# Performance work log

Measured on AMD Instinct MI355X. Metric: run time of the kernel, lower is better.

Reference implementation:

```python
import jax, jax.numpy as jnp
import numpy as np


def phi(x):
    return jax.nn.elu(x) + 1.0


def setup_inputs() -> dict:
    key = jax.random.key(0)
    ks = jax.random.split(key, 6)
    B, C, H, W = 16, 256, 64, 64
    scale = 1.0 / np.sqrt(C)
    x = jax.random.normal(ks[0], (B, C, H, W), dtype=jnp.float32)
    Wq = jax.random.normal(ks[1], (C, C), dtype=jnp.float32) * scale
    Wk = jax.random.normal(ks[2], (C, C), dtype=jnp.float32) * scale
    Wv = jax.random.normal(ks[3], (C, C), dtype=jnp.float32) * scale
    Wo = jax.random.normal(ks[4], (C, C), dtype=jnp.float32) * scale
    bo = jnp.zeros((C,), dtype=jnp.float32)
    return {"x": x, "Wq": Wq, "Wk": Wk, "Wv": Wv, "Wo": Wo, "bo": bo}


def reference(x, Wq, Wk, Wv, Wo, bo):
    # 1x1 convs == channel matmuls: out[b,o,h,w] = sum_c W[o,c] x[b,c,h,w]
    q = jnp.einsum('oc,bchw->bohw', Wq, x)
    k = jnp.einsum('oc,bchw->bohw', Wk, x)
    v = jnp.einsum('oc,bchw->bohw', Wv, x)
    phi_q, phi_k, phi_v = phi(q), phi(k), phi(v)
    # context matrix per batch: [B, C, C]
    qv = jnp.einsum('bchw,bdhw->bcd', phi_q, phi_v)
    # per-batch 1x1 conv with weight qv[b] applied to phi_k[b]
    attended = jnp.einsum('bcd,bdhw->bchw', qv, phi_k)
    # output projection with bias; dropout is identity at eval
    out = jnp.einsum('oc,bchw->bohw', Wo, attended) + bo[None, :, None, None]
    return out
```

## Files before the change

### kernel.cpp

```cpp
#include <hip/hip_runtime.h>
#include <hip/hip_bf16.h>


typedef short  bf16x8 __attribute__((ext_vector_type(8)));
typedef float  f32x4  __attribute__((ext_vector_type(4)));
typedef unsigned short u16x4 __attribute__((ext_vector_type(4)));

#define NB 16
#define NC 256
#define NN 4096

__device__ __forceinline__ unsigned short f2bf(float f) {
    union { float f; unsigned u; } v; v.f = f;
    unsigned r = v.u + 0x7FFFu + ((v.u >> 16) & 1u);
    return (unsigned short)(r >> 16);
}

__device__ __forceinline__ float phi_act(float v) {
    return v > 0.f ? v + 1.f : __expf(v);
}

__device__ __forceinline__ void gload_lds16(const void* g, void* l) {
    __builtin_amdgcn_global_load_lds(
        (const __attribute__((address_space(1))) void*)g,
        (__attribute__((address_space(3))) void*)l, 16, 0, 0);
}

__device__ __forceinline__ void stage_tile(
    const unsigned short* __restrict__ src, int ld, int kb, char* lds, int t)
{
    const int kslot  = t & 7;
    const int rbase  = t >> 3;
    const int srcOff = (kslot * 16) ^ ((rbase & 7) << 4);
    const int wbase  = (t >> 6) * 1024;
    #pragma unroll
    for (int i = 0; i < 4; ++i) {
        const int r = i * 32 + rbase;
        const char* g = (const char*)(src + (size_t)r * ld + kb) + srcOff;
        gload_lds16(g, lds + i * 4096 + wbase);
    }
}

__device__ __forceinline__ bf16x8 frag_ld(const char* lds, int row, int kbyte) {
    return *(const bf16x8*)(lds + row * 128 + (kbyte ^ ((row & 7) << 4)));
}

template<bool SWAP>
__device__ __forceinline__ void gemm128(
    const unsigned short* __restrict__ A, int lda,
    const unsigned short* __restrict__ BT, int ldb,
    int k0, int nk, char* lsA, char* lsB, f32x4 (&acc)[4][4])
{
    const int t = threadIdx.x;
    const int lane = t & 63;
    const int w  = t >> 6;
    const int wr = (w >> 1) * 64, wc = (w & 1) * 64;
    const int q  = lane >> 4, c15 = lane & 15;

    for (int kt = 0; kt < nk; ++kt) {
        const int kb = k0 + kt * 64;
        if (kt) __syncthreads();
        stage_tile(A,  lda, kb, lsA, t);
        stage_tile(BT, ldb, kb, lsB, t);
        __syncthreads();
        #pragma unroll
        for (int g = 0; g < 2; ++g) {
            const int kbyte = g * 64 + q * 16;
            bf16x8 af[4], bfr[4];
            #pragma unroll
            for (int m = 0; m < 4; ++m) af[m]  = frag_ld(lsA, wr + m * 16 + c15, kbyte);
            #pragma unroll
            for (int n = 0; n < 4; ++n) bfr[n] = frag_ld(lsB, wc + n * 16 + c15, kbyte);
            #pragma unroll
            for (int m = 0; m < 4; ++m)
                #pragma unroll
                for (int n = 0; n < 4; ++n)
                    acc[m][n] = SWAP
                        ? __builtin_amdgcn_mfma_f32_16x16x32_bf16(bfr[n], af[m], acc[m][n], 0, 0, 0)
                        : __builtin_amdgcn_mfma_f32_16x16x32_bf16(af[m], bfr[n], acc[m][n], 0, 0, 0);
        }
    }
}

__global__ __launch_bounds__(256) void k_wconv(
    const float* __restrict__ Wq, const float* __restrict__ Wk,
    const float* __restrict__ Wv, const float* __restrict__ Wo,
    unsigned short* __restrict__ Wqkv, unsigned short* __restrict__ Wob)
{
    int i = blockIdx.x * 256 + threadIdx.x;
    if      (i < 65536)  Wqkv[i] = f2bf(Wq[i]);
    else if (i < 131072) Wqkv[i] = f2bf(Wk[i - 65536]);
    else if (i < 196608) Wqkv[i] = f2bf(Wv[i - 131072]);
    else if (i < 262144) Wob[i - 196608] = f2bf(Wo[i - 196608]);
}

__global__ __launch_bounds__(256) void k_xpose(
    const float* __restrict__ x, unsigned short* __restrict__ xT)
{
    __shared__ float tile[64][68];
    const int b  = blockIdx.z;
    const int n0 = blockIdx.x * 64, c0 = blockIdx.y * 64;
    const int t  = threadIdx.x;
    const float* xp = x + ((size_t)b * NC + c0) * NN + n0;
    const int cc = t >> 4, nq = t & 15;
    #pragma unroll
    for (int j = 0; j < 4; ++j) {
        const int c = j * 16 + cc;
        f32x4 v = *(const f32x4*)(xp + (size_t)c * NN + nq * 4);
        *(f32x4*)&tile[c][nq * 4] = v;
    }
    __syncthreads();
    unsigned short* op = xT + ((size_t)b * NN + n0) * NC + c0;
    const int nn0 = t >> 4, cq = t & 15;
    #pragma unroll
    for (int j = 0; j < 4; ++j) {
        const int nn = j * 16 + nn0;
        u16x4 o;
        #pragma unroll
        for (int ii = 0; ii < 4; ++ii) o[ii] = f2bf(tile[cq * 4 + ii][nn]);
        *(u16x4*)(op + (size_t)nn * NC + cq * 4) = o;
    }
}

__global__ __launch_bounds__(256) void k_proj(
    const unsigned short* __restrict__ Wqkv, const unsigned short* __restrict__ xT,
    unsigned short* __restrict__ phiQ, unsigned short* __restrict__ phiKT,
    unsigned short* __restrict__ phiV)
{
    __shared__ char lds[32768];
    const int bid = blockIdx.x;
    const int nt  = bid & 31;
    const int mt  = (bid >> 5) % 6;
    const int b   = bid / 192;
    const unsigned short* A  = Wqkv + mt * 128 * NC;
    const unsigned short* BT = xT + ((size_t)b * NN + nt * 128) * NC;

    const int lane = threadIdx.x & 63;
    const int w    = threadIdx.x >> 6;
    const int wr   = (w >> 1) * 64, wc = (w & 1) * 64;
    const int q4   = (lane >> 4) * 4, c15 = lane & 15;
    const int p    = mt >> 1;

    f32x4 acc[4][4] = {};
    if (p == 1) {
        gemm128<false>(A, NC, BT, NC, 0, 4, lds, lds + 16384, acc);
        unsigned short* dst = phiKT + (size_t)b * NN * NC;
        const int cb = (mt & 1) * 128 + wr + q4;
        const int nb = nt * 128 + wc + c15;
        #pragma unroll
        for (int m = 0; m < 4; ++m)
            #pragma unroll
            for (int n = 0; n < 4; ++n) {
                u16x4 pk;
                #pragma unroll
                for (int i = 0; i < 4; ++i) pk[i] = f2bf(phi_act(acc[m][n][i]));
                *(u16x4*)(dst + (size_t)(nb + n * 16) * NC + cb + m * 16) = pk;
            }
    } else {
        gemm128<true>(A, NC, BT, NC, 0, 4, lds, lds + 16384, acc);
        unsigned short* dst = (p == 0 ? phiQ : phiV) + (size_t)b * NC * NN;
        const int ob = (mt & 1) * 128 + wr + c15;
        const int nb = nt * 128 + wc + q4;
        #pragma unroll
        for (int m = 0; m < 4; ++m)
            #pragma unroll
            for (int n = 0; n < 4; ++n) {
                u16x4 pk;
                #pragma unroll
                for (int i = 0; i < 4; ++i) pk[i] = f2bf(phi_act(acc[m][n][i]));
                *(u16x4*)(dst + (size_t)(ob + m * 16) * NN + nb + n * 16) = pk;
            }
    }
}

__global__ __launch_bounds__(256) void k_qv(
    const unsigned short* __restrict__ phiQ, const unsigned short* __restrict__ phiV,
    float* __restrict__ qvTp)
{
    __shared__ char lds[32768];
    const int bid = blockIdx.x;
    const int s = bid & 7, nt = (bid >> 3) & 1, mt = (bid >> 4) & 1, b = bid >> 5;
    const unsigned short* A  = phiQ + ((size_t)b * NC + mt * 128) * NN;
    const unsigned short* BT = phiV + ((size_t)b * NC + nt * 128) * NN;
    f32x4 acc[4][4] = {};
    gemm128<false>(A, NN, BT, NN, s * 512, 8, lds, lds + 16384, acc);

    const int lane = threadIdx.x & 63, w = threadIdx.x >> 6;
    const int wr = (w >> 1) * 64, wc = (w & 1) * 64;
    const int q4 = (lane >> 4) * 4, c15 = lane & 15;
    float* dst = qvTp + (((size_t)s * NB + b) << 16);
    const int c0 = mt * 128 + wr + q4;
    const int d0 = nt * 128 + wc + c15;
    #pragma unroll
    for (int m = 0; m < 4; ++m)
        #pragma unroll
        for (int n = 0; n < 4; ++n)
            *(f32x4*)(dst + (size_t)(d0 + n * 16) * NC + c0 + m * 16) = acc[m][n];
}

__global__ __launch_bounds__(256) void k_qvred(
    const float* __restrict__ p, unsigned short* __restrict__ qvT)
{
    const size_t i = (size_t)blockIdx.x * 256 + threadIdx.x;
    const f32x4* pv = (const f32x4*)p;
    f32x4 v = pv[i];
    #pragma unroll
    for (int s = 1; s < 8; ++s) v = v + pv[i + (size_t)s * 262144];
    u16x4 o;
    #pragma unroll
    for (int j = 0; j < 4; ++j) o[j] = f2bf(v[j]);
    ((u16x4*)qvT)[i] = o;
}

__global__ __launch_bounds__(256) void k_mproj(
    const unsigned short* __restrict__ Wob, const unsigned short* __restrict__ qvT,
    unsigned short* __restrict__ Mb)
{
    __shared__ char lds[32768];
    const int bid = blockIdx.x;
    const int nt = bid & 1, mt = (bid >> 1) & 1, b = bid >> 2;
    const unsigned short* A  = Wob + mt * 128 * NC;
    const unsigned short* BT = qvT + ((size_t)b << 16) + nt * 128 * NC;
    f32x4 acc[4][4] = {};
    gemm128<true>(A, NC, BT, NC, 0, 4, lds, lds + 16384, acc);

    const int lane = threadIdx.x & 63, w = threadIdx.x >> 6;
    const int wr = (w >> 1) * 64, wc = (w & 1) * 64;
    const int q4 = (lane >> 4) * 4, c15 = lane & 15;
    unsigned short* dst = Mb + ((size_t)b << 16);
    const int ob = mt * 128 + wr + c15;
    const int db = nt * 128 + wc + q4;
    #pragma unroll
    for (int m = 0; m < 4; ++m)
        #pragma unroll
        for (int n = 0; n < 4; ++n) {
            u16x4 pk;
            #pragma unroll
            for (int i = 0; i < 4; ++i) pk[i] = f2bf(acc[m][n][i]);
            *(u16x4*)(dst + (size_t)(ob + m * 16) * NC + db + n * 16) = pk;
        }
}

__global__ __launch_bounds__(256) void k_out(
    const unsigned short* __restrict__ Mb, const unsigned short* __restrict__ phiKT,
    const float* __restrict__ bo, float* __restrict__ out)
{
    __shared__ char lds[32768];
    const int bid = blockIdx.x;
    const int nt = bid & 31, mt = (bid >> 5) & 1, b = bid >> 6;
    const unsigned short* A  = Mb + ((size_t)b << 16) + mt * 128 * NC;
    const unsigned short* BT = phiKT + (size_t)b * NN * NC + (size_t)nt * 128 * NC;
    f32x4 acc[4][4] = {};
    gemm128<true>(A, NC, BT, NC, 0, 4, lds, lds + 16384, acc);

    const int lane = threadIdx.x & 63, w = threadIdx.x >> 6;
    const int wr = (w >> 1) * 64, wc = (w & 1) * 64;
    const int q4 = (lane >> 4) * 4, c15 = lane & 15;
    float* dst = out + (size_t)b * NC * NN;
    #pragma unroll
    for (int m = 0; m < 4; ++m) {
        const int o  = mt * 128 + wr + m * 16 + c15;
        const float bb = bo[o];
        #pragma unroll
        for (int n = 0; n < 4; ++n) {
            f32x4 v = acc[m][n];
            #pragma unroll
            for (int i = 0; i < 4; ++i) v[i] += bb;
            *(f32x4*)(dst + (size_t)o * NN + nt * 128 + wc + n * 16 + q4) = v;
        }
    }
}

extern "C" void kernel_launch(void* const* d_in, const int* in_sizes, int n_in,
                              void* d_out, int out_size, void* d_ws, size_t ws_size,
                              hipStream_t stream)
{
    (void)in_sizes; (void)n_in; (void)out_size; (void)ws_size;
    const float* x  = (const float*)d_in[0];
    const float* Wq = (const float*)d_in[1];
    const float* Wk = (const float*)d_in[2];
    const float* Wv = (const float*)d_in[3];
    const float* Wo = (const float*)d_in[4];
    const float* bo = (const float*)d_in[5];
    float* out = (float*)d_out;

    char* ws = (char*)d_ws;
    size_t off = 0;
    auto alloc = [&](size_t bytes) {
        void* p = ws + off;
        off += (bytes + 255) & ~(size_t)255;
        return p;
    };
    unsigned short* xT    = (unsigned short*)alloc((size_t)NB * NN * NC * 2);
    unsigned short* phiQ  = (unsigned short*)alloc((size_t)NB * NC * NN * 2);
    unsigned short* phiV  = (unsigned short*)alloc((size_t)NB * NC * NN * 2);
    unsigned short* phiKT = (unsigned short*)alloc((size_t)NB * NN * NC * 2);
    unsigned short* qvT   = (unsigned short*)alloc((size_t)NB * NC * NC * 2);
    unsigned short* Mb    = (unsigned short*)alloc((size_t)NB * NC * NC * 2);
    unsigned short* Wqkv  = (unsigned short*)alloc((size_t)768 * NC * 2);
    unsigned short* Wob   = (unsigned short*)alloc((size_t)NC * NC * 2);
    float* qvTp = (float*)xT;

    k_wconv<<<1024, 256, 0, stream>>>(Wq, Wk, Wv, Wo, Wqkv, Wob);
    k_xpose<<<dim3(NN / 64, NC / 64, NB), dim3(256), 0, stream>>>(x, xT);
    k_proj<<<NB * 6 * 32, 256, 0, stream>>>(Wqkv, xT, phiQ, phiKT, phiV);
    k_qv<<<NB * 2 * 2 * 8, 256, 0, stream>>>(phiQ, phiV, qvTp);
    k_qvred<<<1024, 256, 0, stream>>>(qvTp, qvT);
    k_mproj<<<NB * 2 * 2, 256, 0, stream>>>(Wob, qvT, Mb);
    k_out<<<NB * 2 * 32, 256, 0, stream>>>(Mb, phiKT, bo, out);
}
```

Before: 126.4 us.

## Keep weight tiles in registers and double-buffer LDS staging across GEMM kernels

Adds a GEMM helper that loads the full K=256 A operand (weights or the M matrix) into registers once, then streams several 128-column B tiles through double-buffered LDS, running an epilogue per tile. k_proj is split into separate QV and K kernels, each covering several N tiles per block, and k_out/k_mproj use the same helper. k_qv switches to a double-buffered LDS pipeline so the next tile loads while MFMAs run on the current one. Together these cut redundant A reloads and barrier stalls, at the cost of much higher register use (64 bf16x8 fragments), fewer blocks per launch and a launch_bounds occupancy hint of 2.

```diff
diff --git a/kernel.cpp b/kernel.cpp
--- a/kernel.cpp
+++ b/kernel.cpp
@@ -45,32 +45,92 @@
     return *(const bf16x8*)(lds + row * 128 + (kbyte ^ ((row & 7) << 4)));
 }
 
+template<bool SWAP, int G, class Epi>
+__device__ __forceinline__ void gemm_k256_regA(
+    const unsigned short* __restrict__ A,
+    const unsigned short* __restrict__ BT0, int ldb,
+    char* lds, Epi epi)
+{
+    const int t = threadIdx.x, lane = t & 63, w = t >> 6;
+    const int wr = (w >> 1) * 64, wc = (w & 1) * 64;
+    const int q = lane >> 4, c15 = lane & 15;
+
+    bf16x8 af[8][4];
+    {
+        const unsigned short* ab = A + (size_t)(wr + c15) * NC + q * 8;
+        #pragma unroll
+        for (int kg = 0; kg < 8; ++kg)
+            #pragma unroll
+            for (int m = 0; m < 4; ++m)
+                af[kg][m] = *(const bf16x8*)(ab + m * 16 * NC + kg * 32);
+    }
+
+    stage_tile(BT0, ldb, 0, lds, t);
+    f32x4 acc[4][4] = {};
+    for (int nti = 0; nti < G; ++nti) {
+        const unsigned short* BT = BT0 + (size_t)nti * 128 * ldb;
+        #pragma unroll
+        for (int kt = 0; kt < 4; ++kt) {
+            __syncthreads();
+            if (kt < 3)
+                stage_tile(BT, ldb, (kt + 1) * 64, lds + ((kt + 1) & 1) * 16384, t);
+            else if (nti + 1 < G)
+                stage_tile(BT + 128 * ldb, ldb, 0, lds + ((kt + 1) & 1) * 16384, t);
+            const char* cur = lds + (kt & 1) * 16384;
+            #pragma unroll
+            for (int g = 0; g < 2; ++g) {
+                bf16x8 bfr[4];
+                #pragma unroll
+                for (int n = 0; n < 4; ++n)
+                    bfr[n] = frag_ld(cur, wc + n * 16 + c15, g * 64 + q * 16);
+                #pragma unroll
+                for (int m = 0; m < 4; ++m)
+                    #pragma unroll
+                    for (int n = 0; n < 4; ++n)
+                        acc[m][n] = SWAP
+                            ? __builtin_amdgcn_mfma_f32_16x16x32_bf16(bfr[n], af[kt * 2 + g][m], acc[m][n], 0, 0, 0)
+                            : __builtin_amdgcn_mfma_f32_16x16x32_bf16(af[kt * 2 + g][m], bfr[n], acc[m][n], 0, 0, 0);
+            }
+            if (kt == 3) {
+                epi(nti, acc);
+                #pragma unroll
+                for (int m = 0; m < 4; ++m)
+                    #pragma unroll
+                    for (int n = 0; n < 4; ++n)
+                        acc[m][n] = f32x4{0.f, 0.f, 0.f, 0.f};
+            }
+        }
+    }
+}
+
 template<bool SWAP>
-__device__ __forceinline__ void gemm128(
+__device__ __forceinline__ void gemm128_db(
     const unsigned short* __restrict__ A, int lda,
     const unsigned short* __restrict__ BT, int ldb,
-    int k0, int nk, char* lsA, char* lsB, f32x4 (&acc)[4][4])
-{
-    const int t = threadIdx.x;
-    const int lane = t & 63;
-    const int w  = t >> 6;
-    const int wr = (w >> 1) * 64, wc = (w & 1) * 64;
-    const int q  = lane >> 4, c15 = lane & 15;
-
+    int k0, int nk, char* lds, f32x4 (&acc)[4][4])
+{
+    const int t = threadIdx.x, lane = t & 63, w = t >> 6;
+    const int wr = (w >> 1) * 64, wc = (w & 1) * 64;
+    const int q = lane >> 4, c15 = lane & 15;
+
+    stage_tile(A,  lda, k0, lds, t);
+    stage_tile(BT, ldb, k0, lds + 16384, t);
     for (int kt = 0; kt < nk; ++kt) {
-        const int kb = k0 + kt * 64;
-        if (kt) __syncthreads();
-        stage_tile(A,  lda, kb, lsA, t);
-        stage_tile(BT, ldb, kb, lsB, t);
         __syncthreads();
+        if (kt + 1 < nk) {
+            char* nxt = lds + ((kt + 1) & 1) * 32768;
+            stage_tile(A,  lda, k0 + (kt + 1) * 64, nxt, t);
+            stage_tile(BT, ldb, k0 + (kt + 1) * 64, nxt + 16384, t);
+        }
+        const char* cur = lds + (kt & 1) * 32768;
         #pragma unroll
         for (int g = 0; g < 2; ++g) {
             const int kbyte = g * 64 + q * 16;
             bf16x8 af[4], bfr[4];
             #pragma unroll
-            for (int m = 0; m < 4; ++m) af[m]  = frag_ld(lsA, wr + m * 16 + c15, kbyte);
-            #pragma unroll
-            for (int n = 0; n < 4; ++n) bfr[n] = frag_ld(lsB, wc + n * 16 + c15, kbyte);
+            for (int m = 0; m < 4; ++m) af[m]  = frag_ld(cur,         wr + m * 16 + c15, kbyte);
+            #pragma unroll
+            for (int n = 0; n < 4; ++n) bfr[n] = frag_ld(cur + 16384, wc + n * 16 + c15, kbyte);
             #pragma unroll
             for (int m = 0; m < 4; ++m)
                 #pragma unroll
@@ -122,68 +182,80 @@
     }
 }
 
-__global__ __launch_bounds__(256) void k_proj(
+__global__ __launch_bounds__(256, 2) void k_projQV(
     const unsigned short* __restrict__ Wqkv, const unsigned short* __restrict__ xT,
-    unsigned short* __restrict__ phiQ, unsigned short* __restrict__ phiKT,
-    unsigned short* __restrict__ phiV)
-{
-    __shared__ char lds[32768];
-    const int bid = blockIdx.x;
-    const int nt  = bid & 31;
-    const int mt  = (bid >> 5) % 6;
-    const int b   = bid / 192;
-    const unsigned short* A  = Wqkv + mt * 128 * NC;
-    const unsigned short* BT = xT + ((size_t)b * NN + nt * 128) * NC;
-
-    const int lane = threadIdx.x & 63;
-    const int w    = threadIdx.x >> 6;
-    const int wr   = (w >> 1) * 64, wc = (w & 1) * 64;
-    const int q4   = (lane >> 4) * 4, c15 = lane & 15;
-    const int p    = mt >> 1;
-
-    f32x4 acc[4][4] = {};
-    if (p == 1) {
-        gemm128<false>(A, NC, BT, NC, 0, 4, lds, lds + 16384, acc);
-        unsigned short* dst = phiKT + (size_t)b * NN * NC;
-        const int cb = (mt & 1) * 128 + wr + q4;
-        const int nb = nt * 128 + wc + c15;
-        #pragma unroll
-        for (int m = 0; m < 4; ++m)
-            #pragma unroll
-            for (int n = 0; n < 4; ++n) {
-                u16x4 pk;
-                #pragma unroll
-                for (int i = 0; i < 4; ++i) pk[i] = f2bf(phi_act(acc[m][n][i]));
-                *(u16x4*)(dst + (size_t)(nb + n * 16) * NC + cb + m * 16) = pk;
-            }
-    } else {
-        gemm128<true>(A, NC, BT, NC, 0, 4, lds, lds + 16384, acc);
-        unsigned short* dst = (p == 0 ? phiQ : phiV) + (size_t)b * NC * NN;
-        const int ob = (mt & 1) * 128 + wr + c15;
-        const int nb = nt * 128 + wc + q4;
-        #pragma unroll
-        for (int m = 0; m < 4; ++m)
-            #pragma unroll
-            for (int n = 0; n < 4; ++n) {
-                u16x4 pk;
-                #pragma unroll
-                for (int i = 0; i < 4; ++i) pk[i] = f2bf(phi_act(acc[m][n][i]));
-                *(u16x4*)(dst + (size_t)(ob + m * 16) * NN + nb + n * 16) = pk;
-            }
-    }
-}
-
-__global__ __launch_bounds__(256) void k_qv(
+    unsigned short* __restrict__ phiQ, unsigned short* __restrict__ phiV)
+{
+    __shared__ __align__(16) char lds[32768];
+    const int bid = blockIdx.x;
+    const int ntg = bid & 7, sq = (bid >> 3) & 3, b = bid >> 5;
+    const int mt  = (sq < 2) ? sq : sq + 2;
+    const unsigned short* A   = Wqkv + (size_t)mt * 128 * NC;
+    const unsigned short* BT0 = xT + ((size_t)b * NN + ntg * 512) * NC;
+    unsigned short* dst = (sq < 2 ? phiQ : phiV) + (size_t)b * NC * NN;
+
+    const int lane = threadIdx.x & 63, w = threadIdx.x >> 6;
+    const int wr = (w >> 1) * 64, wc = (w & 1) * 64;
+    const int q4 = ((lane >> 4) & 3) * 4, c15 = lane & 15;
+    const int ob = (sq & 1) * 128 + wr + c15;
+
+    gemm_k256_regA<true, 4>(A, BT0, NC, lds,
+        [&](int nti, f32x4 (&acc)[4][4]) {
+            const int nb = ntg * 512 + nti * 128 + wc + q4;
+            #pragma unroll
+            for (int m = 0; m < 4; ++m)
+                #pragma unroll
+                for (int n = 0; n < 4; ++n) {
+                    u16x4 pk;
+                    #pragma unroll
+                    for (int i = 0; i < 4; ++i) pk[i] = f2bf(phi_act(acc[m][n][i]));
+                    *(u16x4*)(dst + (size_t)(ob + m * 16) * NN + nb + n * 16) = pk;
+                }
+        });
+}
+
+__global__ __launch_bounds__(256, 2) void k_projK(
+    const unsigned short* __restrict__ Wqkv, const unsigned short* __restrict__ xT,
+    unsigned short* __restrict__ phiKT)
+{
+    __shared__ __align__(16) char lds[32768];
+    const int bid = blockIdx.x;
+    const int ntg = bid & 15, sk = (bid >> 4) & 1, b = bid >> 5;
+    const unsigned short* A   = Wqkv + (size_t)(2 + sk) * 128 * NC;
+    const unsigned short* BT0 = xT + ((size_t)b * NN + ntg * 256) * NC;
+    unsigned short* dst = phiKT + (size_t)b * NN * NC;
+
+    const int lane = threadIdx.x & 63, w = threadIdx.x >> 6;
+    const int wr = (w >> 1) * 64, wc = (w & 1) * 64;
+    const int q4 = ((lane >> 4) & 3) * 4, c15 = lane & 15;
+    const int cb = sk * 128 + wr + q4;
+
+    gemm_k256_regA<false, 2>(A, BT0, NC, lds,
+        [&](int nti, f32x4 (&acc)[4][4]) {
+            const int nb = ntg * 256 + nti * 128 + wc + c15;
+            #pragma unroll
+            for (int m = 0; m < 4; ++m)
+                #pragma unroll
+                for (int n = 0; n < 4; ++n) {
+                    u16x4 pk;
+                    #pragma unroll
+                    for (int i = 0; i < 4; ++i) pk[i] = f2bf(phi_act(acc[m][n][i]));
+                    *(u16x4*)(dst + (size_t)(nb + n * 16) * NC + cb + m * 16) = pk;
+                }
+        });
+}
+
+__global__ __launch_bounds__(256, 2) void k_qv(
     const unsigned short* __restrict__ phiQ, const unsigned short* __restrict__ phiV,
     float* __restrict__ qvTp)
 {
-    __shared__ char lds[32768];
+    __shared__ __align__(16) char lds[65536];
     const int bid = blockIdx.x;
     const int s = bid & 7, nt = (bid >> 3) & 1, mt = (bid >> 4) & 1, b = bid >> 5;
     const unsigned short* A  = phiQ + ((size_t)b * NC + mt * 128) * NN;
     const unsigned short* BT = phiV + ((size_t)b * NC + nt * 128) * NN;
     f32x4 acc[4][4] = {};
-    gemm128<false>(A, NN, BT, NN, s * 512, 8, lds, lds + 16384, acc);
+    gemm128_db<false>(A, NN, BT, NN, s * 512, 8, lds, acc);
 
     const int lane = threadIdx.x & 63, w = threadIdx.x >> 6;
     const int wr = (w >> 1) * 64, wc = (w & 1) * 64;
@@ -212,63 +284,67 @@
     ((u16x4*)qvT)[i] = o;
 }
 
-__global__ __launch_bounds__(256) void k_mproj(
+__global__ __launch_bounds__(256, 2) void k_mproj(
     const unsigned short* __restrict__ Wob, const unsigned short* __restrict__ qvT,
     unsigned short* __restrict__ Mb)
 {
-    __shared__ char lds[32768];
+    __shared__ __align__(16) char lds[32768];
     const int bid = blockIdx.x;
     const int nt = bid & 1, mt = (bid >> 1) & 1, b = bid >> 2;
-    const unsigned short* A  = Wob + mt * 128 * NC;
-    const unsigned short* BT = qvT + ((size_t)b << 16) + nt * 128 * NC;
-    f32x4 acc[4][4] = {};
-    gemm128<true>(A, NC, BT, NC, 0, 4, lds, lds + 16384, acc);
-
-    const int lane = threadIdx.x & 63, w = threadIdx.x >> 6;
-    const int wr = (w >> 1) * 64, wc = (w & 1) * 64;
-    const int q4 = (lane >> 4) * 4, c15 = lane & 15;
+    const unsigned short* A   = Wob + (size_t)mt * 128 * NC;
+    const unsigned short* BT0 = qvT + ((size_t)b << 16) + (size_t)nt * 128 * NC;
     unsigned short* dst = Mb + ((size_t)b << 16);
+
+    const int lane = threadIdx.x & 63, w = threadIdx.x >> 6;
+    const int wr = (w >> 1) * 64, wc = (w & 1) * 64;
+    const int q4 = ((lane >> 4) & 3) * 4, c15 = lane & 15;
     const int ob = mt * 128 + wr + c15;
     const int db = nt * 128 + wc + q4;
-    #pragma unroll
-    for (int m = 0; m < 4; ++m)
-        #pragma unroll
-        for (int n = 0; n < 4; ++n) {
-            u16x4 pk;
-            #pragma unroll
-            for (int i = 0; i < 4; ++i) pk[i] = f2bf(acc[m][n][i]);
-            *(u16x4*)(dst + (size_t)(ob + m * 16) * NC + db + n * 16) = pk;
-        }
-}
-
-__global__ __launch_bounds__(256) void k_out(
+
+    gemm_k256_regA<true, 1>(A, BT0, NC, lds,
+        [&](int, f32x4 (&acc)[4][4]) {
+            #pragma unroll
+            for (int m = 0; m < 4; ++m)
+                #pragma unroll
+                for (int n = 0; n < 4; ++n) {
+                    u16x4 pk;
+                    #pragma unroll
+                    for (int i = 0; i < 4; ++i) pk[i] = f2bf(acc[m][n][i]);
+                    *(u16x4*)(dst + (size_t)(ob + m * 16) * NC + db + n * 16) = pk;
+                }
+        });
+}
+
+__global__ __launch_bounds__(256, 2) void k_out(
     const unsigned short* __restrict__ Mb, const unsigned short* __restrict__ phiKT,
     const float* __restrict__ bo, float* __restrict__ out)
 {
-    __shared__ char lds[32768];
-    const int bid = blockIdx.x;
-    const int nt = bid & 31, mt = (bid >> 5) & 1, b = bid >> 6;
-    const unsigned short* A  = Mb + ((size_t)b << 16) + mt * 128 * NC;
-    const unsigned short* BT = phiKT + (size_t)b * NN * NC + (size_t)nt * 128 * NC;
-    f32x4 acc[4][4] = {};
-    gemm128<true>(A, NC, BT, NC, 0, 4, lds, lds + 16384, acc);
-
-    const int lane = threadIdx.x & 63, w = threadIdx.x >> 6;
-    const int wr = (w >> 1) * 64, wc = (w & 1) * 64;
-    const int q4 = (lane >> 4) * 4, c15 = lane & 15;
+    __shared__ __align__(16) char lds[32768];
+    const int bid = blockIdx.x;
+    const int ntg = bid & 15, mt = (bid >> 4) & 1, b = bid >> 5;
+    const unsigned short* A   = Mb + ((size_t)b << 16) + (size_t)mt * 128 * NC;
+    const unsigned short* BT0 = phiKT + (size_t)b * NN * NC + (size_t)ntg * 256 * NC;
     float* dst = out + (size_t)b * NC * NN;
-    #pragma unroll
-    for (int m = 0; m < 4; ++m) {
-        const int o  = mt * 128 + wr + m * 16 + c15;
-        const float bb = bo[o];
-        #pragma unroll
-        for (int n = 0; n < 4; ++n) {
-            f32x4 v = acc[m][n];
-            #pragma unroll
-            for (int i = 0; i < 4; ++i) v[i] += bb;
-            *(f32x4*)(dst + (size_t)o * NN + nt * 128 + wc + n * 16 + q4) = v;
-        }
-    }
+
+    const int lane = threadIdx.x & 63, w = threadIdx.x >> 6;
+    const int wr = (w >> 1) * 64, wc = (w & 1) * 64;
+    const int q4 = ((lane >> 4) & 3) * 4, c15 = lane & 15;
+
+    gemm_k256_regA<true, 2>(A, BT0, NC, lds,
+        [&](int nti, f32x4 (&acc)[4][4]) {
+            #pragma unroll
+            for (int m = 0; m < 4; ++m) {
+                const int o = mt * 128 + wr + m * 16 + c15;
+                const float bb = bo[o];
+                #pragma unroll
+                for (int n = 0; n < 4; ++n) {
+                    f32x4 v = acc[m][n];
+                    #pragma unroll
+                    for (int i = 0; i < 4; ++i) v[i] += bb;
+                    *(f32x4*)(dst + (size_t)o * NN + ntg * 256 + nti * 128 + wc + n * 16 + q4) = v;
+                }
+            }
+        });
 }
 
 extern "C" void kernel_launch(void* const* d_in, const int* in_sizes, int n_in,
@@ -303,9 +379,10 @@
 
     k_wconv<<<1024, 256, 0, stream>>>(Wq, Wk, Wv, Wo, Wqkv, Wob);
     k_xpose<<<dim3(NN / 64, NC / 64, NB), dim3(256), 0, stream>>>(x, xT);
-    k_proj<<<NB * 6 * 32, 256, 0, stream>>>(Wqkv, xT, phiQ, phiKT, phiV);
-    k_qv<<<NB * 2 * 2 * 8, 256, 0, stream>>>(phiQ, phiV, qvTp);
+    k_projQV<<<512, 256, 0, stream>>>(Wqkv, xT, phiQ, phiV);
+    k_projK<<<512, 256, 0, stream>>>(Wqkv, xT, phiKT);
+    k_qv<<<512, 256, 0, stream>>>(phiQ, phiV, qvTp);
     k_qvred<<<1024, 256, 0, stream>>>(qvTp, qvT);
-    k_mproj<<<NB * 2 * 2, 256, 0, stream>>>(Wob, qvT, Mb);
-    k_out<<<NB * 2 * 32, 256, 0, stream>>>(Mb, phiKT, bo, out);
-}
+    k_mproj<<<64, 256, 0, stream>>>(Wob, qvT, Mb);
+    k_out<<<512, 256, 0, stream>>>(Mb, phiKT, bo, out);
+}
```

Result: slower. 142.8 us (+13.0%).

## Fuse x transpose and bf16 conversion into projection GEMM B-tile staging

Applied to the files above, without the earlier changes.

Removes the separate transpose kernel that wrote a bf16 xT buffer. The projection GEMM now reads fp32 x directly, converts it to bf16 in registers and writes the transposed, swizzled B tile into LDS. This saves one kernel launch and a full write plus re-read of the transposed activation. In exchange, each of the six projection tiles per batch and column block re-reads fp32 x (twice the bytes of bf16), the B loads become synchronous register loads instead of async global-to-LDS loads, and qvTp now needs its own workspace allocation.

```diff
diff --git a/kernel.cpp b/kernel.cpp
--- a/kernel.cpp
+++ b/kernel.cpp
@@ -43,6 +43,62 @@
 
 __device__ __forceinline__ bf16x8 frag_ld(const char* lds, int row, int kbyte) {
     return *(const bf16x8*)(lds + row * 128 + (kbyte ^ ((row & 7) << 4)));
+}
+
+template<bool SWAP>
+__device__ __forceinline__ void gemm_projx(
+    const unsigned short* __restrict__ A,
+    const float* __restrict__ xb,
+    char* lsA, char* lsB, f32x4 (&acc)[4][4])
+{
+    const int t = threadIdx.x, lane = t & 63, w = t >> 6;
+    const int wr = (w >> 1) * 64, wc = (w & 1) * 64;
+    const int q = lane >> 4, c15 = lane & 15;
+    const int cb = t & 15;
+    const int nb0 = t >> 4;
+
+    for (int kt = 0; kt < 4; ++kt) {
+        const int kb = kt * 64;
+        f32x4 bv[2][4];
+        #pragma unroll
+        for (int i = 0; i < 2; ++i) {
+            const float* src = xb + (size_t)(kb + cb * 4) * NN + (nb0 + 16 * i) * 4;
+            #pragma unroll
+            for (int j = 0; j < 4; ++j)
+                bv[i][j] = *(const f32x4*)(src + (size_t)j * NN);
+        }
+        if (kt) __syncthreads();
+        stage_tile(A, NC, kb, lsA, t);
+        #pragma unroll
+        for (int i = 0; i < 2; ++i) {
+            const int nb = nb0 + 16 * i;
+            #pragma unroll
+            for (int jj = 0; jj < 4; ++jj) {
+                const int n = nb * 4 + jj;
+                u16x4 wv;
+                #pragma unroll
+                for (int j = 0; j < 4; ++j) wv[j] = f2bf(bv[i][j][jj]);
+                *(u16x4*)(lsB + n * 128 + ((cb * 8) ^ ((n & 7) << 4))) = wv;
+            }
+        }
+        __syncthreads();
+        #pragma unroll
+        for (int g = 0; g < 2; ++g) {
+            const int kbyte = g * 64 + q * 16;
+            bf16x8 af[4], bfr[4];
+            #pragma unroll
+            for (int m = 0; m < 4; ++m) af[m]  = frag_ld(lsA, wr + m * 16 + c15, kbyte);
+            #pragma unroll
+            for (int n = 0; n < 4; ++n) bfr[n] = frag_ld(lsB, wc + n * 16 + c15, kbyte);
+            #pragma unroll
+            for (int m = 0; m < 4; ++m)
+                #pragma unroll
+                for (int n = 0; n < 4; ++n)
+                    acc[m][n] = SWAP
+                        ? __builtin_amdgcn_mfma_f32_16x16x32_bf16(bfr[n], af[m], acc[m][n], 0, 0, 0)
+                        : __builtin_amdgcn_mfma_f32_16x16x32_bf16(af[m], bfr[n], acc[m][n], 0, 0, 0);
+        }
+    }
 }
 
 template<bool SWAP>
@@ -82,7 +138,7 @@
     }
 }
 
-__global__ __launch_bounds__(256) void k_wconv(
+__global__ __launch_bounds__(256) void k_wcvt(
     const float* __restrict__ Wq, const float* __restrict__ Wk,
     const float* __restrict__ Wv, const float* __restrict__ Wo,
     unsigned short* __restrict__ Wqkv, unsigned short* __restrict__ Wob)
@@ -94,46 +150,18 @@
     else if (i < 262144) Wob[i - 196608] = f2bf(Wo[i - 196608]);
 }
 
-__global__ __launch_bounds__(256) void k_xpose(
-    const float* __restrict__ x, unsigned short* __restrict__ xT)
-{
-    __shared__ float tile[64][68];
-    const int b  = blockIdx.z;
-    const int n0 = blockIdx.x * 64, c0 = blockIdx.y * 64;
-    const int t  = threadIdx.x;
-    const float* xp = x + ((size_t)b * NC + c0) * NN + n0;
-    const int cc = t >> 4, nq = t & 15;
-    #pragma unroll
-    for (int j = 0; j < 4; ++j) {
-        const int c = j * 16 + cc;
-        f32x4 v = *(const f32x4*)(xp + (size_t)c * NN + nq * 4);
-        *(f32x4*)&tile[c][nq * 4] = v;
-    }
-    __syncthreads();
-    unsigned short* op = xT + ((size_t)b * NN + n0) * NC + c0;
-    const int nn0 = t >> 4, cq = t & 15;
-    #pragma unroll
-    for (int j = 0; j < 4; ++j) {
-        const int nn = j * 16 + nn0;
-        u16x4 o;
-        #pragma unroll
-        for (int ii = 0; ii < 4; ++ii) o[ii] = f2bf(tile[cq * 4 + ii][nn]);
-        *(u16x4*)(op + (size_t)nn * NC + cq * 4) = o;
-    }
-}
-
 __global__ __launch_bounds__(256) void k_proj(
-    const unsigned short* __restrict__ Wqkv, const unsigned short* __restrict__ xT,
+    const unsigned short* __restrict__ Wqkv, const float* __restrict__ x,
     unsigned short* __restrict__ phiQ, unsigned short* __restrict__ phiKT,
     unsigned short* __restrict__ phiV)
 {
-    __shared__ char lds[32768];
+    __shared__ __align__(16) char lds[32768];
     const int bid = blockIdx.x;
     const int nt  = bid & 31;
     const int mt  = (bid >> 5) % 6;
     const int b   = bid / 192;
-    const unsigned short* A  = Wqkv + mt * 128 * NC;
-    const unsigned short* BT = xT + ((size_t)b * NN + nt * 128) * NC;
+    const unsigned short* A = Wqkv + (size_t)mt * 128 * NC;
+    const float* xb = x + (size_t)b * NC * NN + nt * 128;
 
     const int lane = threadIdx.x & 63;
     const int w    = threadIdx.x >> 6;
@@ -143,7 +171,7 @@
 
     f32x4 acc[4][4] = {};
     if (p == 1) {
-        gemm128<false>(A, NC, BT, NC, 0, 4, lds, lds + 16384, acc);
+        gemm_projx<false>(A, xb, lds, lds + 16384, acc);
         unsigned short* dst = phiKT + (size_t)b * NN * NC;
         const int cb = (mt & 1) * 128 + wr + q4;
         const int nb = nt * 128 + wc + c15;
@@ -157,7 +185,7 @@
                 *(u16x4*)(dst + (size_t)(nb + n * 16) * NC + cb + m * 16) = pk;
             }
     } else {
-        gemm128<true>(A, NC, BT, NC, 0, 4, lds, lds + 16384, acc);
+        gemm_projx<true>(A, xb, lds, lds + 16384, acc);
         unsigned short* dst = (p == 0 ? phiQ : phiV) + (size_t)b * NC * NN;
         const int ob = (mt & 1) * 128 + wr + c15;
         const int nb = nt * 128 + wc + q4;
@@ -291,21 +319,19 @@
         off += (bytes + 255) & ~(size_t)255;
         return p;
     };
-    unsigned short* xT    = (unsigned short*)alloc((size_t)NB * NN * NC * 2);
     unsigned short* phiQ  = (unsigned short*)alloc((size_t)NB * NC * NN * 2);
     unsigned short* phiV  = (unsigned short*)alloc((size_t)NB * NC * NN * 2);
     unsigned short* phiKT = (unsigned short*)alloc((size_t)NB * NN * NC * 2);
+    float*          qvTp  = (float*)alloc((size_t)8 * NB * NC * NC * 4);
     unsigned short* qvT   = (unsigned short*)alloc((size_t)NB * NC * NC * 2);
     unsigned short* Mb    = (unsigned short*)alloc((size_t)NB * NC * NC * 2);
     unsigned short* Wqkv  = (unsigned short*)alloc((size_t)768 * NC * 2);
     unsigned short* Wob   = (unsigned short*)alloc((size_t)NC * NC * 2);
-    float* qvTp = (float*)xT;
-
-    k_wconv<<<1024, 256, 0, stream>>>(Wq, Wk, Wv, Wo, Wqkv, Wob);
-    k_xpose<<<dim3(NN / 64, NC / 64, NB), dim3(256), 0, stream>>>(x, xT);
-    k_proj<<<NB * 6 * 32, 256, 0, stream>>>(Wqkv, xT, phiQ, phiKT, phiV);
-    k_qv<<<NB * 2 * 2 * 8, 256, 0, stream>>>(phiQ, phiV, qvTp);
+
+    k_wcvt<<<1024, 256, 0, stream>>>(Wq, Wk, Wv, Wo, Wqkv, Wob);
+    k_proj<<<3072, 256, 0, stream>>>(Wqkv, x, phiQ, phiKT, phiV);
+    k_qv<<<512, 256, 0, stream>>>(phiQ, phiV, qvTp);
     k_qvred<<<1024, 256, 0, stream>>>(qvTp, qvT);
-    k_mproj<<<NB * 2 * 2, 256, 0, stream>>>(Wob, qvT, Mb);
-    k_out<<<NB * 2 * 32, 256, 0, stream>>>(Mb, phiKT, bo, out);
-}
+    k_mproj<<<64, 256, 0, stream>>>(Wob, qvT, Mb);
+    k_out<<<1024, 256, 0, stream>>>(Mb, phiKT, bo, out);
+}
```

Result: slower. 146.8 us (+16.1%).
